# Kernel tuning notes

Measured on AMD Instinct MI355X. Metric: run time of the kernel, lower is better.

Reference implementation:

```python
import jax, jax.numpy as jnp
import numpy as np

D_MODEL = 768
D_STATE = 16
D_CONV = 4
EXPAND = 2
D_IN = D_MODEL // 2          # per-direction model dim = 384
D_INNER = EXPAND * D_IN      # ssm inner dim = 768
DT_RANK = (D_IN + 15) // 16  # 24 (mamba 'auto')
B, L = 2, 2048
EPS = 1e-5


def silu(x):
    return x * jax.nn.sigmoid(x)


def layernorm(x, w, b):
    m = jnp.mean(x, axis=-1, keepdims=True)
    v = jnp.var(x, axis=-1, keepdims=True)
    return (x - m) * jax.lax.rsqrt(v + EPS) * w + b


def causal_conv1d(u, w, b):
    # u: (B,L,di), w: (di,K) depthwise causal conv, b: (di,)
    K = w.shape[1]
    up = jnp.pad(u, ((0, 0), (K - 1, 0), (0, 0)))
    Lq = u.shape[1]
    y = sum(up[:, k:k + Lq, :] * w[:, k] for k in range(K))
    return y + b


def mamba_ssm(u, in_w, in_b, conv_w, conv_b, xp_w, dt_w, dt_b, A_log, Dp, out_w, out_b):
    # u: (B,L,D_IN)
    Bz = u.shape[0]
    xz = u @ in_w + in_b                         # (B,L,2*D_INNER)
    x, z = jnp.split(xz, 2, axis=-1)             # (B,L,D_INNER) each
    x = silu(causal_conv1d(x, conv_w, conv_b))
    xd = x @ xp_w                                # (B,L,DT_RANK+2N)
    dt = jax.nn.softplus(xd[..., :DT_RANK] @ dt_w + dt_b)   # (B,L,D_INNER)
    Bm = xd[..., DT_RANK:DT_RANK + D_STATE]      # (B,L,N)
    Cm = xd[..., DT_RANK + D_STATE:]             # (B,L,N)
    A = -jnp.exp(A_log)                          # (D_INNER,N)

    def step(h, xs):
        dt_t, x_t, B_t, C_t = xs                 # (B,di),(B,di),(B,N),(B,N)
        h = jnp.exp(dt_t[..., None] * A) * h + (dt_t * x_t)[..., None] * B_t[:, None, :]
        y = jnp.einsum('bdn,bn->bd', h, C_t)
        return h, y

    h0 = jnp.zeros((Bz, D_INNER, D_STATE), x.dtype)
    xs = (dt.transpose(1, 0, 2), x.transpose(1, 0, 2),
          Bm.transpose(1, 0, 2), Cm.transpose(1, 0, 2))
    _, ys = jax.lax.scan(step, h0, xs)           # ys: (L,B,D_INNER)
    y = ys.transpose(1, 0, 2) + x * Dp
    y = y * silu(z)
    return y @ out_w + out_b                     # (B,L,D_IN)


def setup_inputs() -> dict:
    key = jax.random.key(0)

    def nrm(i, shape, s=0.02):
        return jax.random.normal(jax.random.fold_in(key, i), shape, jnp.float32) * s

    d = {"x": jax.random.normal(jax.random.fold_in(key, 0), (B, L, D_MODEL), jnp.float32)}
    d["in_norm_w"] = jnp.ones(D_MODEL); d["in_norm_b"] = jnp.zeros(D_MODEL)
    d["ip_w"] = nrm(1, (D_MODEL, 2 * D_IN)); d["ip_b"] = jnp.zeros(2 * D_IN)
    i = 10
    for p in ("f", "b"):
        d[p + "_in_w"] = nrm(i, (D_IN, 2 * D_INNER)); d[p + "_in_b"] = jnp.zeros(2 * D_INNER)
        d[p + "_conv_w"] = nrm(i + 1, (D_INNER, D_CONV), 0.2); d[p + "_conv_b"] = jnp.zeros(D_INNER)
        d[p + "_xp_w"] = nrm(i + 2, (D_INNER, DT_RANK + 2 * D_STATE))
        d[p + "_dt_w"] = nrm(i + 3, (DT_RANK, D_INNER), 0.1)
        d[p + "_dt_b"] = nrm(i + 4, (D_INNER,), 0.5)
        d[p + "_A_log"] = jnp.log(jnp.tile(jnp.arange(1, D_STATE + 1, dtype=jnp.float32), (D_INNER, 1)))
        d[p + "_D"] = jnp.ones(D_INNER)
        d[p + "_out_w"] = nrm(i + 5, (D_INNER, D_IN)); d[p + "_out_b"] = jnp.zeros(D_IN)
        i += 10
    d["op_w"] = nrm(30, (2 * D_IN, D_MODEL)); d["op_b"] = jnp.zeros(D_MODEL)
    d["norm_w"] = jnp.ones(D_MODEL); d["norm_b"] = jnp.zeros(D_MODEL)
    return d


def reference(x, in_norm_w, in_norm_b, ip_w, ip_b,
              f_in_w, f_in_b, f_conv_w, f_conv_b, f_xp_w, f_dt_w, f_dt_b, f_A_log, f_D, f_out_w, f_out_b,
              b_in_w, b_in_b, b_conv_w, b_conv_b, b_xp_w, b_dt_w, b_dt_b, b_A_log, b_D, b_out_w, b_out_b,
              op_w, op_b, norm_w, norm_b):
    residual = x
    xn = layernorm(x, in_norm_w, in_norm_b)
    xp = xn @ ip_w + ip_b                        # (B,L,2*D_IN)
    x_fwd, x_bwd = jnp.split(xp, 2, axis=-1)
    out_fwd = mamba_ssm(x_fwd, f_in_w, f_in_b, f_conv_w, f_conv_b, f_xp_w,
                        f_dt_w, f_dt_b, f_A_log, f_D, f_out_w, f_out_b)
    out_bwd = mamba_ssm(jnp.flip(x_bwd, axis=1), b_in_w, b_in_b, b_conv_w, b_conv_b, b_xp_w,
                        b_dt_w, b_dt_b, b_A_log, b_D, b_out_w, b_out_b)
    out_bwd = jnp.flip(out_bwd, axis=1)
    out = jnp.concatenate([out_fwd, out_bwd], axis=-1) @ op_w + op_b
    # dropout is identity in eval mode
    return layernorm(residual + out, norm_w, norm_b)
```

## Files before the change

kernel.cpp:

```cpp
#include <hip/hip_runtime.h>
#include <hip/hip_bf16.h>
#include <math.h>
#include <type_traits>

#define BATCH 2
#define SEQ   2048
#define DMODEL 768
#define DIN   384
#define DINNER 768
#define DSTATE 16
#define DTRANK 24
#define ROWS  (BATCH*SEQ)
#define NCH   64
#define CLEN  (SEQ/NCH)

using short8  = __attribute__((ext_vector_type(8))) short;
using floatx4 = __attribute__((ext_vector_type(4))) float;

__device__ __forceinline__ ushort f2bf(float f) {
    union { float f; uint u; } v; v.f = f;
    uint r = (v.u + 0x7fffu + ((v.u >> 16) & 1u)) >> 16;
    return (ushort)r;
}
__device__ __forceinline__ float bf2f(ushort h) {
    union { uint u; float f; } v; v.u = ((uint)h) << 16;
    return v.f;
}
__device__ __forceinline__ void async16(const ushort* g, ushort* l) {
    __builtin_amdgcn_global_load_lds(
        (const __attribute__((address_space(1))) void*)g,
        (__attribute__((address_space(3))) void*)l,
        16, 0, 0);
}

template<int TM, int TN> struct GemmShT { ushort lA[TM * 64]; ushort lB[TN * 64]; };

template<int TM, int TN>
__device__ __forceinline__ void gemm_accum(
    const ushort* __restrict__ A, int lda,
    const ushort* __restrict__ Bt, int ldb,
    int K, int m0, int n0, GemmShT<TM, TN>& sh,
    floatx4 (&acc)[TM / 32][TN / 32])
{
    constexpr int WM = TM / 2, WN = TN / 2;
    constexpr int MT = WM / 16, NT = WN / 16;
    constexpr int AI = TM / 32, BI = TN / 32;
    const int tid = threadIdx.x;
    const int wave = tid >> 6, lane = tid & 63;
    const int wm = wave >> 1, wn = wave & 1;
    const int quad = lane >> 4, l16 = lane & 15;
    const int lrow = lane >> 3;
    const int lcol = ((lane & 7) ^ (lane >> 3)) * 8;

    for (int k0 = 0; k0 < K; k0 += 64) {
#pragma unroll
        for (int i = 0; i < AI; i++) {
            int rb = (wave * AI + i) * 8;
            async16(A + (size_t)(m0 + rb + lrow) * lda + k0 + lcol, &sh.lA[rb * 64]);
        }
#pragma unroll
        for (int i = 0; i < BI; i++) {
            int rb = (wave * BI + i) * 8;
            async16(Bt + (size_t)(n0 + rb + lrow) * ldb + k0 + lcol, &sh.lB[rb * 64]);
        }
        __syncthreads();
#pragma unroll
        for (int ks = 0; ks < 2; ks++) {
            short8 af[MT], bf[NT];
#pragma unroll
            for (int i = 0; i < MT; i++) {
                int row = wm * WM + i * 16 + l16;
                af[i] = *(const short8*)&sh.lA[row * 64 + ((ks * 4 + quad) ^ (row & 7)) * 8];
            }
#pragma unroll
            for (int j = 0; j < NT; j++) {
                int row = wn * WN + j * 16 + l16;
                bf[j] = *(const short8*)&sh.lB[row * 64 + ((ks * 4 + quad) ^ (row & 7)) * 8];
            }
#pragma unroll
            for (int i = 0; i < MT; i++)
#pragma unroll
                for (int j = 0; j < NT; j++)
                    acc[i][j] = __builtin_amdgcn_mfma_f32_16x16x32_bf16(af[i], bf[j], acc[i][j], 0, 0, 0);
        }
        __syncthreads();
    }
}

template<int TM, int TN, bool OUT_BF>
__device__ __forceinline__ void gemm_epilogue(
    const float* __restrict__ bias, void* __restrict__ C, int ldc, int N,
    int m0, int n0, floatx4 (&acc)[TM / 32][TN / 32])
{
    constexpr int WM = TM / 2, WN = TN / 2;
    constexpr int MT = WM / 16, NT = WN / 16;
    const int tid = threadIdx.x;
    const int wave = tid >> 6, lane = tid & 63;
    const int wm = wave >> 1, wn = wave & 1;
    const int quad = lane >> 4, l16 = lane & 15;
#pragma unroll
    for (int i = 0; i < MT; i++) {
#pragma unroll
        for (int j = 0; j < NT; j++) {
            int row = m0 + wm * WM + i * 16 + quad * 4;
            int col = n0 + wn * WN + j * 16 + l16;
            if (col < N) {
                float bv = bias ? bias[col] : 0.f;
#pragma unroll
                for (int r = 0; r < 4; r++) {
                    float v = acc[i][j][r] + bv;
                    if (OUT_BF) ((ushort*)C)[(size_t)(row + r) * ldc + col] = f2bf(v);
                    else        ((float*)C)[(size_t)(row + r) * ldc + col] = v;
                }
            }
        }
    }
}

template<int TM, int TN, bool OUT_BF>
__global__ __launch_bounds__(256) void mfma_gemm_k(
    const ushort* __restrict__ A0, const ushort* __restrict__ A1, int lda,
    const ushort* __restrict__ B0, const ushort* __restrict__ B1, int ldb,
    const float* __restrict__ bias0, const float* __restrict__ bias1,
    void* __restrict__ C0, void* __restrict__ C1, int ldc, int N, int K)
{
    __shared__ GemmShT<TM, TN> sh;
    const ushort* A  = blockIdx.z ? A1 : A0;
    const ushort* Bt = blockIdx.z ? B1 : B0;
    const float* bias = blockIdx.z ? bias1 : bias0;
    void* C = blockIdx.z ? C1 : C0;
    floatx4 acc[TM / 32][TN / 32];
#pragma unroll
    for (int i = 0; i < TM / 32; i++)
#pragma unroll
        for (int j = 0; j < TN / 32; j++)
            acc[i][j] = (floatx4){0.f, 0.f, 0.f, 0.f};
    int m0 = blockIdx.y * TM, n0 = blockIdx.x * TN;
    gemm_accum<TM, TN>(A, lda, Bt, ldb, K, m0, n0, sh, acc);
    gemm_epilogue<TM, TN, OUT_BF>(bias, C, ldc, N, m0, n0, acc);
}

__global__ __launch_bounds__(256) void xddt_kernel(
    const ushort* __restrict__ xcf, const ushort* __restrict__ xcb,
    const ushort* __restrict__ Wcf, const ushort* __restrict__ Wcb,
    const float* __restrict__ dtbf, const float* __restrict__ dtbb,
    float* __restrict__ xdf, float* __restrict__ xdb,
    float* __restrict__ dtf, float* __restrict__ dtb)
{
    constexpr int TM = 128, TN = 64;
    __shared__ GemmShT<TM, TN> sh;
    const ushort* A  = blockIdx.z ? xcb : xcf;
    const ushort* Bt = blockIdx.z ? Wcb : Wcf;
    const float* dbias = blockIdx.z ? dtbb : dtbf;
    float* xd = blockIdx.z ? xdb : xdf;
    float* dt = blockIdx.z ? dtb : dtf;
    floatx4 acc[4][2];
#pragma unroll
    for (int i = 0; i < 4; i++)
#pragma unroll
        for (int j = 0; j < 2; j++)
            acc[i][j] = (floatx4){0.f, 0.f, 0.f, 0.f};
    int m0 = blockIdx.y * TM, n0 = blockIdx.x * TN;
    gemm_accum<TM, TN>(A, 768, Bt, 768, 768, m0, n0, sh, acc);
    const int tid = threadIdx.x;
    const int wave = tid >> 6, lane = tid & 63;
    const int wm = wave >> 1, wn = wave & 1;
    const int quad = lane >> 4, l16 = lane & 15;
#pragma unroll
    for (int i = 0; i < 4; i++) {
#pragma unroll
        for (int j = 0; j < 2; j++) {
            int row = m0 + wm * 64 + i * 16 + quad * 4;
            int col = n0 + wn * 32 + j * 16 + l16;
            if (col < 56) {
#pragma unroll
                for (int r = 0; r < 4; r++)
                    xd[(size_t)(row + r) * 56 + col] = acc[i][j][r];
            } else if (col >= 64) {
                int jj = col - 64;
                float bv = dbias[jj];
#pragma unroll
                for (int r = 0; r < 4; r++) {
                    float v = acc[i][j][r] + bv;
                    v = (v > 20.f) ? v : log1pf(__expf(v));
                    dt[(size_t)(row + r) * 768 + jj] = v;
                }
            }
        }
    }
}

template<int TM, int TN>
__global__ __launch_bounds__(256) void outop_kernel(
    const ushort* __restrict__ A0, const ushort* __restrict__ B0,
    const ushort* __restrict__ A1, const ushort* __restrict__ B1,
    const float* __restrict__ bias, float* __restrict__ C,
    int lda, int ldb, int ldc, int N, int K)
{
    __shared__ GemmShT<TM, TN> sh;
    floatx4 acc[TM / 32][TN / 32];
#pragma unroll
    for (int i = 0; i < TM / 32; i++)
#pragma unroll
        for (int j = 0; j < TN / 32; j++)
            acc[i][j] = (floatx4){0.f, 0.f, 0.f, 0.f};
    int m0 = blockIdx.y * TM, n0 = blockIdx.x * TN;
    gemm_accum<TM, TN>(A0, lda, B0, ldb, K, m0, n0, sh, acc);
    gemm_accum<TM, TN>(A1, lda, B1, ldb, K, m0, n0, sh, acc);
    gemm_epilogue<TM, TN, false>(bias, (void*)C, ldc, N, m0, n0, acc);
}

struct LnSh { float ss[4]; float ssq[4]; float m; float rs; };

template<bool OUT_BF>
__device__ __forceinline__ void ln_row(
    int row, const float* __restrict__ x, const float* __restrict__ res,
    const float* __restrict__ w, const float* __restrict__ b,
    void* __restrict__ out, LnSh& sh)
{
    int tid = threadIdx.x;
    const float* xr = x + (size_t)row * DMODEL;
    const float* rr = res ? res + (size_t)row * DMODEL : nullptr;
    float v[3];
    float s = 0.f, sq = 0.f;
#pragma unroll
    for (int j = 0; j < 3; j++) {
        int i = tid + j * 256;
        float val = xr[i];
        if (rr) val += rr[i];
        v[j] = val; s += val; sq += val * val;
    }
#pragma unroll
    for (int off = 32; off; off >>= 1) {
        s  += __shfl_down(s,  off);
        sq += __shfl_down(sq, off);
    }
    int wid = tid >> 6;
    if ((tid & 63) == 0) { sh.ss[wid] = s; sh.ssq[wid] = sq; }
    __syncthreads();
    if (tid == 0) {
        float S  = sh.ss[0] + sh.ss[1] + sh.ss[2] + sh.ss[3];
        float SQ = sh.ssq[0] + sh.ssq[1] + sh.ssq[2] + sh.ssq[3];
        float m  = S * (1.0f / DMODEL);
        float var = SQ * (1.0f / DMODEL) - m * m;
        sh.m = m;
        sh.rs = rsqrtf(var + 1e-5f);
    }
    __syncthreads();
    float m = sh.m, rs = sh.rs;
#pragma unroll
    for (int j = 0; j < 3; j++) {
        int i = tid + j * 256;
        float r = (v[j] - m) * rs * w[i] + b[i];
        if (OUT_BF) ((ushort*)out)[(size_t)row * DMODEL + i] = f2bf(r);
        else        ((float*)out)[(size_t)row * DMODEL + i] = r;
    }
}

__global__ __launch_bounds__(256) void ln2_kernel(
    const float* __restrict__ x, const float* __restrict__ res,
    const float* __restrict__ w, const float* __restrict__ b,
    float* __restrict__ out)
{
    __shared__ LnSh sh;
    ln_row<false>(blockIdx.x, x, res, w, b, (void*)out, sh);
}

struct TD { const float* src; ushort* dst; int K, N, Kp, Np, ldd, tile0, tkp, mode; };
struct PrepArgs {
    TD d[12];
    int ntc;
    const float *x, *in_nw, *in_nb;
    ushort* xn;
};

__global__ __launch_bounds__(256) void prep_kernel(PrepArgs p)
{
    __shared__ union { float tile[32][33]; LnSh l; } sh;
    int bi = blockIdx.x;
    if (bi < p.ntc) {
        int i = 0;
        while (i < 11 && bi >= p.d[i + 1].tile0) i++;
        TD t = p.d[i];
        int local = bi - t.tile0;
        int tki = local % t.tkp, tn = local / t.tkp;
        int k0 = tki * 32, n0 = tn * 32;
        if (t.mode == 0) {
            int tx = threadIdx.x & 31, ty = threadIdx.x >> 5;
#pragma unroll
            for (int r = ty; r < 32; r += 8) {
                int k = k0 + r, n = n0 + tx;
                sh.tile[r][tx] = (k < t.K && n < t.N) ? t.src[(size_t)k * t.N + n] : 0.f;
            }
            __syncthreads();
#pragma unroll
            for (int r = ty; r < 32; r += 8) {
                int n = n0 + r, k = k0 + tx;
                t.dst[(size_t)n * t.ldd + k] = f2bf(sh.tile[tx][r]);
            }
        } else {
#pragma unroll
            for (int e = threadIdx.x; e < 1024; e += 256) {
                int r = e >> 5, c = e & 31;
                int k = k0 + r, n = n0 + c;
                float v = (k < t.K && n < t.N) ? t.src[(size_t)k * t.N + n] : 0.f;
                t.dst[(size_t)k * t.ldd + n] = f2bf(v);
            }
        }
    } else {
        ln_row<true>(bi - p.ntc, p.x, (const float*)nullptr, p.in_nw, p.in_nb,
                     (void*)p.xn, sh.l);
    }
}

struct WfArgs {
    const ushort *fin, *bin, *opT, *ipc, *fow, *bow;
    const ushort *dtwTf, *dtwTb, *xpcf, *xpcb;
    ushort *WzF, *WzB, *WoF, *WoB, *WcF, *WcB;
    const float *ip_b, *f_in_b, *b_in_b, *f_out_b, *b_out_b, *op_b;
    const float *f_in_w32, *b_in_w32, *op_w32;
    float *bzf, *bzb, *bo;
};

__global__ __launch_bounds__(256) void wfuse_kernel(WfArgs p)
{
    __shared__ GemmShT<128, 64> sh;
    int t = blockIdx.x;
    if (t < 576) {
        const ushort *A, *Bt; ushort* C; int lda, ldb, K, m0, n0;
        if (t < 144)      { A = p.fin;   lda = 384; Bt = p.ipc;       ldb = 768; K = 384; C = p.WzF;           int u = t;       m0 = (u / 12) * 128; n0 = (u % 12) * 64; }
        else if (t < 288) { A = p.bin;   lda = 384; Bt = p.ipc + 384; ldb = 768; K = 384; C = p.WzB;           int u = t - 144; m0 = (u / 12) * 128; n0 = (u % 12) * 64; }
        else if (t < 360) { A = p.opT;   lda = 768; Bt = p.fow;       ldb = 384; K = 384; C = p.WoF;           int u = t - 288; m0 = (u / 12) * 128; n0 = (u % 12) * 64; }
        else if (t < 432) { A = p.opT + 384; lda = 768; Bt = p.bow;   ldb = 384; K = 384; C = p.WoB;           int u = t - 360; m0 = (u / 12) * 128; n0 = (u % 12) * 64; }
        else if (t < 504) { A = p.dtwTf; lda = 64;  Bt = p.xpcf;      ldb = 64;  K = 64;  C = p.WcF + 64*768;  int u = t - 432; m0 = (u / 12) * 128; n0 = (u % 12) * 64; }
        else              { A = p.dtwTb; lda = 64;  Bt = p.xpcb;      ldb = 64;  K = 64;  C = p.WcB + 64*768;  int u = t - 504; m0 = (u / 12) * 128; n0 = (u % 12) * 64; }
        floatx4 acc[4][2];
#pragma unroll
        for (int i = 0; i < 4; i++)
#pragma unroll
            for (int j = 0; j < 2; j++)
                acc[i][j] = (floatx4){0.f, 0.f, 0.f, 0.f};
        gemm_accum<128, 64>(A, lda, Bt, ldb, K, m0, n0, sh, acc);
        gemm_epilogue<128, 64, true>((const float*)nullptr, (void*)C, 768, 768, m0, n0, acc);
    } else if (t < 582) {
        int n = (t - 576) * 256 + threadIdx.x;
        float acc = p.f_in_b[n];
        for (int j = 0; j < 384; j++)
            acc = fmaf(p.ip_b[j], p.f_in_w32[(size_t)j * 1536 + n], acc);
        p.bzf[n] = acc;
    } else if (t < 588) {
        int n = (t - 582) * 256 + threadIdx.x;
        float acc = p.b_in_b[n];
        for (int j = 0; j < 384; j++)
            acc = fmaf(p.ip_b[384 + j], p.b_in_w32[(size_t)j * 1536 + n], acc);
        p.bzb[n] = acc;
    } else {
        int n = (t - 588) * 256 + threadIdx.x;
        float acc = p.op_b[n];
        for (int j = 0; j < 384; j++)
            acc = fmaf(p.f_out_b[j], p.op_w32[(size_t)j * 768 + n], acc);
        for (int j = 0; j < 384; j++)
            acc = fmaf(p.b_out_b[j], p.op_w32[(size_t)(384 + j) * 768 + n], acc);
        p.bo[n] = acc;
    }
}

__global__ __launch_bounds__(256) void conv_silu_kernel(
    const ushort* __restrict__ xzf, const ushort* __restrict__ xzb,
    const float* __restrict__ cwf, const float* __restrict__ cbf,
    const float* __restrict__ cwb, const float* __restrict__ cbb,
    ushort* __restrict__ outf, ushort* __restrict__ outb)
{
    int rev = blockIdx.y;
    const ushort* xz = rev ? xzb : xzf;
    const float* cw = rev ? cwb : cwf;
    const float* cb = rev ? cbb : cbf;
    ushort* out = rev ? outb : outf;

    int idx = blockIdx.x * 256 + threadIdx.x;
    int d = idx % DINNER;
    int row = idx / DINNER;
    int t = row & (SEQ - 1), b = row >> 11;
    float4 w4 = *(const float4*)&cw[d * 4];
    float wk[4] = {w4.x, w4.y, w4.z, w4.w};
    float acc = cb[d];
#pragma unroll
    for (int k = 0; k < 4; k++) {
        int ts = rev ? (t + 3 - k) : (t - 3 + k);
        if (ts >= 0 && ts < SEQ)
            acc = fmaf(wk[k], bf2f(xz[((size_t)(b * SEQ + ts)) * 1536 + d]), acc);
    }
    float sig = 1.f / (1.f + __expf(-acc));
    out[idx] = f2bf(acc * sig);
}

template<bool FULL>
__global__ __launch_bounds__(256) void scan_chunk_kernel(
    const float* __restrict__ dtf, const ushort* __restrict__ xcf,
    const float* __restrict__ xdf, const ushort* __restrict__ xzf,
    const float* __restrict__ Alf, const float* __restrict__ Dff,
    const float* __restrict__ dtb, const ushort* __restrict__ xcb,
    const float* __restrict__ xdb, const ushort* __restrict__ xzb,
    const float* __restrict__ Alb, const float* __restrict__ Dbb,
    float* __restrict__ Hloc, float* __restrict__ Wp,
    const float* __restrict__ Hin,
    ushort* __restrict__ yf, ushort* __restrict__ yb)
{
    const int d     = blockIdx.x * 256 + threadIdx.x;
    const int chunk = blockIdx.y;
    const int bz    = blockIdx.z;
    const int dir   = bz >> 1;
    const int bat   = bz & 1;

    const float*  dt = dir ? dtb : dtf;
    const ushort* xc = dir ? xcb : xcf;
    const float*  xd = dir ? xdb : xdf;
    const ushort* xz = dir ? xzb : xzf;
    const float*  Al = dir ? Alb : Alf;
    const float*  Dp = dir ? Dbb : Dff;
    ushort* yo = dir ? yb : yf;

    float a[16];
    {
        const float4* Ap = (const float4*)(Al + (size_t)d * 16);
#pragma unroll
        for (int q = 0; q < 4; q++) {
            float4 v = Ap[q];
            a[q*4+0] = -__expf(v.x); a[q*4+1] = -__expf(v.y);
            a[q*4+2] = -__expf(v.z); a[q*4+3] = -__expf(v.w);
        }
    }
    const float a0 = a[0];
    bool fast = true;
#pragma unroll
    for (int n = 0; n < 16; n++) {
        float ideal = a0 * (float)(n + 1);
        fast = fast && (fabsf(a[n] - ideal) <= 1e-4f * fabsf(ideal) + 1e-7f);
    }

    float h[16];
    if (FULL) {
        size_t base = ((size_t)(bz * NCH + chunk) * DINNER + d) * 16;
#pragma unroll
        for (int q = 0; q < 4; q++) {
            float4 v = *(const float4*)(Hin + base + q * 4);
            h[q*4+0] = v.x; h[q*4+1] = v.y; h[q*4+2] = v.z; h[q*4+3] = v.w;
        }
    } else {
#pragma unroll
        for (int n = 0; n < 16; n++) h[n] = 0.f;
    }

    const float Dd = FULL ? Dp[d] : 0.f;
    float S = 0.f;

    auto run = [&](auto FASTC) {
        constexpr bool FAST = decltype(FASTC)::value;
#pragma unroll 2
        for (int i = 0; i < CLEN; i++) {
            int tl = chunk * CLEN + i;
            int t  = dir ? (SEQ - 1 - tl) : tl;
            size_t r = (size_t)(bat * SEQ + t);
            float dtv = dt[r * DINNER + d];
            float xv  = bf2f(xc[r * DINNER + d]);
            const float* bp = xd + r * 56 + DTRANK;
            float4 B0 = *(const float4*)(bp + 0);
            float4 B1 = *(const float4*)(bp + 4);
            float4 B2 = *(const float4*)(bp + 8);
            float4 B3 = *(const float4*)(bp + 12);
            float Bv[16] = {B0.x,B0.y,B0.z,B0.w, B1.x,B1.y,B1.z,B1.w,
                            B2.x,B2.y,B2.z,B2.w, B3.x,B3.y,B3.z,B3.w};
            float w[16];
            if (FAST) {
                float e1 = __expf(dtv * a0);
                float e2 = e1*e1, e4 = e2*e2, e8 = e4*e4;
                w[0]=e1;      w[1]=e2;      w[2]=e2*e1;   w[3]=e4;
                w[4]=e4*e1;   w[5]=e4*e2;   w[6]=e4*w[2]; w[7]=e8;
                w[8]=e8*e1;   w[9]=e8*e2;   w[10]=e8*w[2];w[11]=e8*e4;
                w[12]=e8*w[4];w[13]=e8*w[5];w[14]=e8*w[6];w[15]=e8*e8;
            } else {
#pragma unroll
                for (int n = 0; n < 16; n++) w[n] = __expf(dtv * a[n]);
            }
            float bx = dtv * xv;
#pragma unroll
            for (int n = 0; n < 16; n++)
                h[n] = fmaf(w[n], h[n], bx * Bv[n]);
            S += dtv;
            if (FULL) {
                const float* cp = bp + DSTATE;
                float4 C0 = *(const float4*)(cp + 0);
                float4 C1 = *(const float4*)(cp + 4);
                float4 C2 = *(const float4*)(cp + 8);
                float4 C3 = *(const float4*)(cp + 12);
                float Cv[16] = {C0.x,C0.y,C0.z,C0.w, C1.x,C1.y,C1.z,C1.w,
                                C2.x,C2.y,C2.z,C2.w, C3.x,C3.y,C3.z,C3.w};
                float y = 0.f;
#pragma unroll
                for (int n = 0; n < 16; n++) y = fmaf(h[n], Cv[n], y);
                float zv = bf2f(xz[r * 1536 + DINNER + d]);
                float sig = 1.f / (1.f + __expf(-zv));
                yo[r * DINNER + d] = f2bf((y + xv * Dd) * (zv * sig));
            }
        }
    };
    if (fast) run(std::true_type{}); else run(std::false_type{});

    if (!FULL) {
        float W[16];
        if (fast) {
            float E1 = __expf(S * a0);
            float E2 = E1*E1, E4 = E2*E2, E8 = E4*E4;
            W[0]=E1;      W[1]=E2;      W[2]=E2*E1;   W[3]=E4;
            W[4]=E4*E1;   W[5]=E4*E2;   W[6]=E4*W[2]; W[7]=E8;
            W[8]=E8*E1;   W[9]=E8*E2;   W[10]=E8*W[2];W[11]=E8*E4;
            W[12]=E8*W[4];W[13]=E8*W[5];W[14]=E8*W[6];W[15]=E8*E8;
        } else {
#pragma unroll
            for (int n = 0; n < 16; n++) W[n] = __expf(S * a[n]);
        }
        size_t base = ((size_t)(bz * NCH + chunk) * DINNER + d) * 16;
#pragma unroll
        for (int q = 0; q < 4; q++) {
            *(float4*)(Hloc + base + q*4) = make_float4(h[q*4+0], h[q*4+1], h[q*4+2], h[q*4+3]);
            *(float4*)(Wp   + base + q*4) = make_float4(W[q*4+0], W[q*4+1], W[q*4+2], W[q*4+3]);
        }
    }
}

__global__ __launch_bounds__(256) void scan_combine(
    const float* __restrict__ Hloc, const float* __restrict__ Wp,
    float* __restrict__ Hin)
{
    int idx = blockIdx.x * 256 + threadIdx.x;
    int bz = idx / (DINNER * 16);
    int rest = idx % (DINNER * 16);
    float hin = 0.f;
#pragma unroll 4
    for (int k = 0; k < NCH; k++) {
        size_t o = (size_t)(bz * NCH + k) * (DINNER * 16) + rest;
        Hin[o] = hin;
        hin = fmaf(Wp[o], hin, Hloc[o]);
    }
}

extern "C" void kernel_launch(void* const* d_in, const int* in_sizes, int n_in,
                              void* d_out, int out_size, void* d_ws, size_t ws_size,
                              hipStream_t stream)
{
    const float* x        = (const float*)d_in[0];
    const float* in_nw    = (const float*)d_in[1];
    const float* in_nb    = (const float*)d_in[2];
    const float* ip_w     = (const float*)d_in[3];
    const float* ip_b     = (const float*)d_in[4];
    const float* f_in_w   = (const float*)d_in[5];
    const float* f_in_b   = (const float*)d_in[6];
    const float* f_conv_w = (const float*)d_in[7];
    const float* f_conv_b = (const float*)d_in[8];
    const float* f_xp_w   = (const float*)d_in[9];
    const float* f_dt_w   = (const float*)d_in[10];
    const float* f_dt_b   = (const float*)d_in[11];
    const float* f_A_log  = (const float*)d_in[12];
    const float* f_D      = (const float*)d_in[13];
    const float* f_out_w  = (const float*)d_in[14];
    const float* f_out_b  = (const float*)d_in[15];
    const float* b_in_w   = (const float*)d_in[16];
    const float* b_in_b   = (const float*)d_in[17];
    const float* b_conv_w = (const float*)d_in[18];
    const float* b_conv_b = (const float*)d_in[19];
    const float* b_xp_w   = (const float*)d_in[20];
    const float* b_dt_w   = (const float*)d_in[21];
    const float* b_dt_b   = (const float*)d_in[22];
    const float* b_A_log  = (const float*)d_in[23];
    const float* b_D      = (const float*)d_in[24];
    const float* b_out_w  = (const float*)d_in[25];
    const float* b_out_b  = (const float*)d_in[26];
    const float* op_w     = (const float*)d_in[27];
    const float* op_b     = (const float*)d_in[28];
    const float* norm_w   = (const float*)d_in[29];
    const float* norm_b   = (const float*)d_in[30];

    size_t off = 0;
    auto alloc = [&](size_t bytes) {
        void* p = (char*)d_ws + off;
        off += (bytes + 255) & ~(size_t)255;
        return p;
    };
    const size_t R = ROWS;
    ushort* xn_bf   = (ushort*)alloc(R * 768 * 2);
    ushort* xz_f_bf = (ushort*)alloc(R * 1536 * 2);
    ushort* xz_b_bf = (ushort*)alloc(R * 1536 * 2);
    ushort* xc_f_bf = (ushort*)alloc(R * 768 * 2);
    ushort* xc_b_bf = (ushort*)alloc(R * 768 * 2);
    float*  xd_f    = (float*)alloc(R * 56 * 4);
    float*  xd_b    = (float*)alloc(R * 56 * 4);
    float*  dt_f    = (float*)alloc(R * 768 * 4);
    float*  dt_b    = (float*)alloc(R * 768 * 4);
    ushort* y_f_bf  = (ushort*)alloc(R * 768 * 2);
    ushort* y_b_bf  = (ushort*)alloc(R * 768 * 2);
    float*  outraw  = (float*)alloc(R * 768 * 4);
    const size_t SCN = (size_t)4 * NCH * DINNER * 16;
    float* Hloc = (float*)alloc(SCN * 4);
    float* Wpb  = (float*)alloc(SCN * 4);
    float* Hin  = (float*)alloc(SCN * 4);
    ushort* Wt_fin = (ushort*)alloc((size_t)1536 * 384 * 2);
    ushort* Wt_bin = (ushort*)alloc((size_t)1536 * 384 * 2);
    ushort* Wt_op  = (ushort*)alloc((size_t)768 * 768 * 2);
    ushort* ipc    = (ushort*)alloc((size_t)768 * 768 * 2);
    ushort* fow    = (ushort*)alloc((size_t)768 * 384 * 2);
    ushort* bow    = (ushort*)alloc((size_t)768 * 384 * 2);
    ushort* dtwT_f = (ushort*)alloc((size_t)768 * 64 * 2);
    ushort* dtwT_b = (ushort*)alloc((size_t)768 * 64 * 2);
    ushort* xpc_f  = (ushort*)alloc((size_t)768 * 64 * 2);
    ushort* xpc_b  = (ushort*)alloc((size_t)768 * 64 * 2);
    ushort* WzF    = (ushort*)alloc((size_t)1536 * 768 * 2);
    ushort* WzB    = (ushort*)alloc((size_t)1536 * 768 * 2);
    ushort* WoF    = (ushort*)alloc((size_t)768 * 768 * 2);
    ushort* WoB    = (ushort*)alloc((size_t)768 * 768 * 2);
    ushort* WcF    = (ushort*)alloc((size_t)832 * 768 * 2);
    ushort* WcB    = (ushort*)alloc((size_t)832 * 768 * 2);
    float*  bzf    = (float*)alloc(1536 * 4);
    float*  bzb    = (float*)alloc(1536 * 4);
    float*  bo     = (float*)alloc(768 * 4);

    PrepArgs pa;
    int tile0 = 0, nd = 0;
    auto add = [&](const float* s, ushort* dst, int K, int N, int Kp, int Np,
                   int ldd, int mode) {
        pa.d[nd] = TD{s, dst, K, N, Kp, Np, ldd, tile0, Kp / 32, mode};
        tile0 += (Kp / 32) * (Np / 32);
        nd++;
    };
    add(f_in_w,  Wt_fin,      384, 1536, 384, 1536, 384, 0);
    add(b_in_w,  Wt_bin,      384, 1536, 384, 1536, 384, 0);
    add(op_w,    Wt_op,       768, 768,  768, 768,  768, 0);
    add(f_xp_w,  WcF,         768, 56,   768, 64,   768, 0);
    add(b_xp_w,  WcB,         768, 56,   768, 64,   768, 0);
    add(f_dt_w,  dtwT_f,      24,  768,  64,  768,  64,  0);
    add(b_dt_w,  dtwT_b,      24,  768,  64,  768,  64,  0);
    add(ip_w,    ipc,         768, 768,  768, 768,  768, 1);
    add(f_out_w, fow,         768, 384,  768, 384,  384, 1);
    add(b_out_w, bow,         768, 384,  768, 384,  384, 1);
    add(f_xp_w,  xpc_f,       768, 56,   768, 64,   64,  1);
    add(b_xp_w,  xpc_b,       768, 56,   768, 64,   64,  1);
    pa.ntc = tile0;
    pa.x = x; pa.in_nw = in_nw; pa.in_nb = in_nb; pa.xn = xn_bf;
    hipLaunchKernelGGL(prep_kernel, dim3(tile0 + ROWS), dim3(256), 0, stream, pa);

    WfArgs wa;
    wa.fin = Wt_fin; wa.bin = Wt_bin; wa.opT = Wt_op;
    wa.ipc = ipc; wa.fow = fow; wa.bow = bow;
    wa.dtwTf = dtwT_f; wa.dtwTb = dtwT_b; wa.xpcf = xpc_f; wa.xpcb = xpc_b;
    wa.WzF = WzF; wa.WzB = WzB; wa.WoF = WoF; wa.WoB = WoB; wa.WcF = WcF; wa.WcB = WcB;
    wa.ip_b = ip_b; wa.f_in_b = f_in_b; wa.b_in_b = b_in_b;
    wa.f_out_b = f_out_b; wa.b_out_b = b_out_b; wa.op_b = op_b;
    wa.f_in_w32 = f_in_w; wa.b_in_w32 = b_in_w; wa.op_w32 = op_w;
    wa.bzf = bzf; wa.bzb = bzb; wa.bo = bo;
    hipLaunchKernelGGL(wfuse_kernel, dim3(591), dim3(256), 0, stream, wa);

    hipLaunchKernelGGL((mfma_gemm_k<128, 128, true>), dim3(12, 32, 2), dim3(256), 0, stream,
                       xn_bf, xn_bf, 768, WzF, WzB, 768, bzf, bzb,
                       (void*)xz_f_bf, (void*)xz_b_bf, 1536, 1536, 768);

    hipLaunchKernelGGL(conv_silu_kernel, dim3(ROWS * DINNER / 256, 2), dim3(256), 0, stream,
                       xz_f_bf, xz_b_bf, f_conv_w, f_conv_b, b_conv_w, b_conv_b,
                       xc_f_bf, xc_b_bf);

    hipLaunchKernelGGL(xddt_kernel, dim3(13, 32, 2), dim3(256), 0, stream,
                       xc_f_bf, xc_b_bf, WcF, WcB, f_dt_b, b_dt_b,
                       xd_f, xd_b, dt_f, dt_b);

    hipLaunchKernelGGL((scan_chunk_kernel<false>), dim3(DINNER / 256, NCH, 4), dim3(256), 0, stream,
                       dt_f, xc_f_bf, xd_f, xz_f_bf, f_A_log, f_D,
                       dt_b, xc_b_bf, xd_b, xz_b_bf, b_A_log, b_D,
                       Hloc, Wpb, (const float*)nullptr, (ushort*)nullptr, (ushort*)nullptr);
    hipLaunchKernelGGL(scan_combine, dim3(4 * DINNER * 16 / 256), dim3(256), 0, stream,
                       Hloc, Wpb, Hin);
    hipLaunchKernelGGL((scan_chunk_kernel<true>), dim3(DINNER / 256, NCH, 4), dim3(256), 0, stream,
                       dt_f, xc_f_bf, xd_f, xz_f_bf, f_A_log, f_D,
                       dt_b, xc_b_bf, xd_b, xz_b_bf, b_A_log, b_D,
                       (float*)nullptr, (float*)nullptr, Hin, y_f_bf, y_b_bf);

    hipLaunchKernelGGL((outop_kernel<128, 64>), dim3(12, 32), dim3(256), 0, stream,
                       y_f_bf, WoF, y_b_bf, WoB, bo, outraw, 768, 768, 768, 768, 768);

    hipLaunchKernelGGL(ln2_kernel, dim3(ROWS), dim3(256), 0, stream,
                       x, outraw, norm_w, norm_b, (float*)d_out);
}
```

Before: 364.9 us.

## Unfuse x_proj and dt_proj into two GEMMs with bf16 intermediate

The earlier code pre-multiplied dt_w into x_proj weights (a 768x768 folded matrix per direction) so one K=768 GEMM produced both xd and dt. Now x_proj runs as its own small GEMM (N=64) writing bf16 xd, and a separate K=64 GEMM computes dt from it with a numerically stable softplus. This removes the large folded-weight precompute and cuts the main GEMM's work from about 832x768 to 64x768 plus 768x64 per row. In exchange it adds a kernel launch, routes dt through a bf16-rounded intermediate, and has the scan read B and C as bf16, which lowers precision.

```diff
diff --git a/kernel.cpp b/kernel.cpp
--- a/kernel.cpp
+++ b/kernel.cpp
@@ -32,6 +32,11 @@
         (__attribute__((address_space(3))) void*)l,
         16, 0, 0);
 }
+__device__ __forceinline__ float softplus_fast(float v) {
+    if (v > 20.f) return v;
+    float e = __expf(-fabsf(v));
+    return fmaxf(v, 0.f) + __logf(1.f + e);
+}
 
 template<int TM, int TN> struct GemmShT { ushort lA[TM * 64]; ushort lB[TN * 64]; };
 
@@ -140,20 +145,18 @@
     gemm_epilogue<TM, TN, OUT_BF>(bias, C, ldc, N, m0, n0, acc);
 }
 
-__global__ __launch_bounds__(256) void xddt_kernel(
-    const ushort* __restrict__ xcf, const ushort* __restrict__ xcb,
-    const ushort* __restrict__ Wcf, const ushort* __restrict__ Wcb,
+__global__ __launch_bounds__(256) void dt_kernel(
+    const ushort* __restrict__ xdf, const ushort* __restrict__ xdb,
+    const ushort* __restrict__ dtwTf, const ushort* __restrict__ dtwTb,
     const float* __restrict__ dtbf, const float* __restrict__ dtbb,
-    float* __restrict__ xdf, float* __restrict__ xdb,
     float* __restrict__ dtf, float* __restrict__ dtb)
 {
     constexpr int TM = 128, TN = 64;
     __shared__ GemmShT<TM, TN> sh;
-    const ushort* A  = blockIdx.z ? xcb : xcf;
-    const ushort* Bt = blockIdx.z ? Wcb : Wcf;
-    const float* dbias = blockIdx.z ? dtbb : dtbf;
-    float* xd = blockIdx.z ? xdb : xdf;
-    float* dt = blockIdx.z ? dtb : dtf;
+    const ushort* A  = blockIdx.z ? xdb : xdf;
+    const ushort* Bt = blockIdx.z ? dtwTb : dtwTf;
+    const float* bias = blockIdx.z ? dtbb : dtbf;
+    float* C = blockIdx.z ? dtb : dtf;
     floatx4 acc[4][2];
 #pragma unroll
     for (int i = 0; i < 4; i++)
@@ -161,7 +164,7 @@
         for (int j = 0; j < 2; j++)
             acc[i][j] = (floatx4){0.f, 0.f, 0.f, 0.f};
     int m0 = blockIdx.y * TM, n0 = blockIdx.x * TN;
-    gemm_accum<TM, TN>(A, 768, Bt, 768, 768, m0, n0, sh, acc);
+    gemm_accum<TM, TN>(A, 64, Bt, 64, 64, m0, n0, sh, acc);
     const int tid = threadIdx.x;
     const int wave = tid >> 6, lane = tid & 63;
     const int wm = wave >> 1, wn = wave & 1;
@@ -172,20 +175,10 @@
         for (int j = 0; j < 2; j++) {
             int row = m0 + wm * 64 + i * 16 + quad * 4;
             int col = n0 + wn * 32 + j * 16 + l16;
-            if (col < 56) {
-#pragma unroll
-                for (int r = 0; r < 4; r++)
-                    xd[(size_t)(row + r) * 56 + col] = acc[i][j][r];
-            } else if (col >= 64) {
-                int jj = col - 64;
-                float bv = dbias[jj];
-#pragma unroll
-                for (int r = 0; r < 4; r++) {
-                    float v = acc[i][j][r] + bv;
-                    v = (v > 20.f) ? v : log1pf(__expf(v));
-                    dt[(size_t)(row + r) * 768 + jj] = v;
-                }
-            }
+            float bv = bias[col];
+#pragma unroll
+            for (int r = 0; r < 4; r++)
+                C[(size_t)(row + r) * 768 + col] = softplus_fast(acc[i][j][r] + bv);
         }
     }
 }
@@ -315,8 +308,7 @@
 
 struct WfArgs {
     const ushort *fin, *bin, *opT, *ipc, *fow, *bow;
-    const ushort *dtwTf, *dtwTb, *xpcf, *xpcb;
-    ushort *WzF, *WzB, *WoF, *WoB, *WcF, *WcB;
+    ushort *WzF, *WzB, *WoF, *WoB;
     const float *ip_b, *f_in_b, *b_in_b, *f_out_b, *b_out_b, *op_b;
     const float *f_in_w32, *b_in_w32, *op_w32;
     float *bzf, *bzb, *bo;
@@ -326,36 +318,34 @@
 {
     __shared__ GemmShT<128, 64> sh;
     int t = blockIdx.x;
-    if (t < 576) {
-        const ushort *A, *Bt; ushort* C; int lda, ldb, K, m0, n0;
-        if (t < 144)      { A = p.fin;   lda = 384; Bt = p.ipc;       ldb = 768; K = 384; C = p.WzF;           int u = t;       m0 = (u / 12) * 128; n0 = (u % 12) * 64; }
-        else if (t < 288) { A = p.bin;   lda = 384; Bt = p.ipc + 384; ldb = 768; K = 384; C = p.WzB;           int u = t - 144; m0 = (u / 12) * 128; n0 = (u % 12) * 64; }
-        else if (t < 360) { A = p.opT;   lda = 768; Bt = p.fow;       ldb = 384; K = 384; C = p.WoF;           int u = t - 288; m0 = (u / 12) * 128; n0 = (u % 12) * 64; }
-        else if (t < 432) { A = p.opT + 384; lda = 768; Bt = p.bow;   ldb = 384; K = 384; C = p.WoB;           int u = t - 360; m0 = (u / 12) * 128; n0 = (u % 12) * 64; }
-        else if (t < 504) { A = p.dtwTf; lda = 64;  Bt = p.xpcf;      ldb = 64;  K = 64;  C = p.WcF + 64*768;  int u = t - 432; m0 = (u / 12) * 128; n0 = (u % 12) * 64; }
-        else              { A = p.dtwTb; lda = 64;  Bt = p.xpcb;      ldb = 64;  K = 64;  C = p.WcB + 64*768;  int u = t - 504; m0 = (u / 12) * 128; n0 = (u % 12) * 64; }
+    if (t < 432) {
+        const ushort *A, *Bt; ushort* C; int lda, ldb, m0, n0;
+        if (t < 144)      { A = p.fin;       lda = 384; Bt = p.ipc;       ldb = 768; C = p.WzF; int u = t;       m0 = (u / 12) * 128; n0 = (u % 12) * 64; }
+        else if (t < 288) { A = p.bin;       lda = 384; Bt = p.ipc + 384; ldb = 768; C = p.WzB; int u = t - 144; m0 = (u / 12) * 128; n0 = (u % 12) * 64; }
+        else if (t < 360) { A = p.opT;       lda = 768; Bt = p.fow;       ldb = 384; C = p.WoF; int u = t - 288; m0 = (u / 12) * 128; n0 = (u % 12) * 64; }
+        else              { A = p.opT + 384; lda = 768; Bt = p.bow;       ldb = 384; C = p.WoB; int u = t - 360; m0 = (u / 12) * 128; n0 = (u % 12) * 64; }
         floatx4 acc[4][2];
 #pragma unroll
         for (int i = 0; i < 4; i++)
 #pragma unroll
             for (int j = 0; j < 2; j++)
                 acc[i][j] = (floatx4){0.f, 0.f, 0.f, 0.f};
-        gemm_accum<128, 64>(A, lda, Bt, ldb, K, m0, n0, sh, acc);
+        gemm_accum<128, 64>(A, lda, Bt, ldb, 384, m0, n0, sh, acc);
         gemm_epilogue<128, 64, true>((const float*)nullptr, (void*)C, 768, 768, m0, n0, acc);
-    } else if (t < 582) {
-        int n = (t - 576) * 256 + threadIdx.x;
+    } else if (t < 438) {
+        int n = (t - 432) * 256 + threadIdx.x;
         float acc = p.f_in_b[n];
         for (int j = 0; j < 384; j++)
             acc = fmaf(p.ip_b[j], p.f_in_w32[(size_t)j * 1536 + n], acc);
         p.bzf[n] = acc;
-    } else if (t < 588) {
-        int n = (t - 582) * 256 + threadIdx.x;
+    } else if (t < 444) {
+        int n = (t - 438) * 256 + threadIdx.x;
         float acc = p.b_in_b[n];
         for (int j = 0; j < 384; j++)
             acc = fmaf(p.ip_b[384 + j], p.b_in_w32[(size_t)j * 1536 + n], acc);
         p.bzb[n] = acc;
     } else {
-        int n = (t - 588) * 256 + threadIdx.x;
+        int n = (t - 444) * 256 + threadIdx.x;
         float acc = p.op_b[n];
         for (int j = 0; j < 384; j++)
             acc = fmaf(p.f_out_b[j], p.op_w32[(size_t)j * 768 + n], acc);
@@ -397,10 +387,10 @@
 template<bool FULL>
 __global__ __launch_bounds__(256) void scan_chunk_kernel(
     const float* __restrict__ dtf, const ushort* __restrict__ xcf,
-    const float* __restrict__ xdf, const ushort* __restrict__ xzf,
+    const ushort* __restrict__ xdf, const ushort* __restrict__ xzf,
     const float* __restrict__ Alf, const float* __restrict__ Dff,
     const float* __restrict__ dtb, const ushort* __restrict__ xcb,
-    const float* __restrict__ xdb, const ushort* __restrict__ xzb,
+    const ushort* __restrict__ xdb, const ushort* __restrict__ xzb,
     const float* __restrict__ Alb, const float* __restrict__ Dbb,
     float* __restrict__ Hloc, float* __restrict__ Wp,
     const float* __restrict__ Hin,
@@ -414,7 +404,7 @@
 
     const float*  dt = dir ? dtb : dtf;
     const ushort* xc = dir ? xcb : xcf;
-    const float*  xd = dir ? xdb : xdf;
+    const ushort* xd = dir ? xdb : xdf;
     const ushort* xz = dir ? xzb : xzf;
     const float*  Al = dir ? Alb : Alf;
     const float*  Dp = dir ? Dbb : Dff;
@@ -463,13 +453,15 @@
             size_t r = (size_t)(bat * SEQ + t);
             float dtv = dt[r * DINNER + d];
             float xv  = bf2f(xc[r * DINNER + d]);
-            const float* bp = xd + r * 56 + DTRANK;
-            float4 B0 = *(const float4*)(bp + 0);
-            float4 B1 = *(const float4*)(bp + 4);
-            float4 B2 = *(const float4*)(bp + 8);
-            float4 B3 = *(const float4*)(bp + 12);
-            float Bv[16] = {B0.x,B0.y,B0.z,B0.w, B1.x,B1.y,B1.z,B1.w,
-                            B2.x,B2.y,B2.z,B2.w, B3.x,B3.y,B3.z,B3.w};
+            const ushort* bp = xd + r * 64 + DTRANK;
+            short8 b0 = *(const short8*)(bp);
+            short8 b1 = *(const short8*)(bp + 8);
+            float Bv[16];
+#pragma unroll
+            for (int n = 0; n < 8; n++) {
+                Bv[n]     = bf2f((ushort)b0[n]);
+                Bv[8 + n] = bf2f((ushort)b1[n]);
+            }
             float w[16];
             if (FAST) {
                 float e1 = __expf(dtv * a0);
@@ -488,13 +480,14 @@
                 h[n] = fmaf(w[n], h[n], bx * Bv[n]);
             S += dtv;
             if (FULL) {
-                const float* cp = bp + DSTATE;
-                float4 C0 = *(const float4*)(cp + 0);
-                float4 C1 = *(const float4*)(cp + 4);
-                float4 C2 = *(const float4*)(cp + 8);
-                float4 C3 = *(const float4*)(cp + 12);
-                float Cv[16] = {C0.x,C0.y,C0.z,C0.w, C1.x,C1.y,C1.z,C1.w,
-                                C2.x,C2.y,C2.z,C2.w, C3.x,C3.y,C3.z,C3.w};
+                short8 c0 = *(const short8*)(bp + 16);
+                short8 c1 = *(const short8*)(bp + 24);
+                float Cv[16];
+#pragma unroll
+                for (int n = 0; n < 8; n++) {
+                    Cv[n]     = bf2f((ushort)c0[n]);
+                    Cv[8 + n] = bf2f((ushort)c1[n]);
+                }
                 float y = 0.f;
 #pragma unroll
                 for (int n = 0; n < 16; n++) y = fmaf(h[n], Cv[n], y);
@@ -592,8 +585,8 @@
     ushort* xz_b_bf = (ushort*)alloc(R * 1536 * 2);
     ushort* xc_f_bf = (ushort*)alloc(R * 768 * 2);
     ushort* xc_b_bf = (ushort*)alloc(R * 768 * 2);
-    float*  xd_f    = (float*)alloc(R * 56 * 4);
-    float*  xd_b    = (float*)alloc(R * 56 * 4);
+    ushort* xd64_f  = (ushort*)alloc(R * 64 * 2);
+    ushort* xd64_b  = (ushort*)alloc(R * 64 * 2);
     float*  dt_f    = (float*)alloc(R * 768 * 4);
     float*  dt_b    = (float*)alloc(R * 768 * 4);
     ushort* y_f_bf  = (ushort*)alloc(R * 768 * 2);
@@ -606,19 +599,17 @@
     ushort* Wt_fin = (ushort*)alloc((size_t)1536 * 384 * 2);
     ushort* Wt_bin = (ushort*)alloc((size_t)1536 * 384 * 2);
     ushort* Wt_op  = (ushort*)alloc((size_t)768 * 768 * 2);
+    ushort* Wt_fxp = (ushort*)alloc((size_t)64 * 768 * 2);
+    ushort* Wt_bxp = (ushort*)alloc((size_t)64 * 768 * 2);
+    ushort* dtwT_f = (ushort*)alloc((size_t)768 * 64 * 2);
+    ushort* dtwT_b = (ushort*)alloc((size_t)768 * 64 * 2);
     ushort* ipc    = (ushort*)alloc((size_t)768 * 768 * 2);
     ushort* fow    = (ushort*)alloc((size_t)768 * 384 * 2);
     ushort* bow    = (ushort*)alloc((size_t)768 * 384 * 2);
-    ushort* dtwT_f = (ushort*)alloc((size_t)768 * 64 * 2);
-    ushort* dtwT_b = (ushort*)alloc((size_t)768 * 64 * 2);
-    ushort* xpc_f  = (ushort*)alloc((size_t)768 * 64 * 2);
-    ushort* xpc_b  = (ushort*)alloc((size_t)768 * 64 * 2);
     ushort* WzF    = (ushort*)alloc((size_t)1536 * 768 * 2);
     ushort* WzB    = (ushort*)alloc((size_t)1536 * 768 * 2);
     ushort* WoF    = (ushort*)alloc((size_t)768 * 768 * 2);
     ushort* WoB    = (ushort*)alloc((size_t)768 * 768 * 2);
-    ushort* WcF    = (ushort*)alloc((size_t)832 * 768 * 2);
-    ushort* WcB    = (ushort*)alloc((size_t)832 * 768 * 2);
     float*  bzf    = (float*)alloc(1536 * 4);
     float*  bzb    = (float*)alloc(1536 * 4);
     float*  bo     = (float*)alloc(768 * 4);
@@ -631,32 +622,30 @@
         tile0 += (Kp / 32) * (Np / 32);
         nd++;
     };
-    add(f_in_w,  Wt_fin,      384, 1536, 384, 1536, 384, 0);
-    add(b_in_w,  Wt_bin,      384, 1536, 384, 1536, 384, 0);
-    add(op_w,    Wt_op,       768, 768,  768, 768,  768, 0);
-    add(f_xp_w,  WcF,         768, 56,   768, 64,   768, 0);
-    add(b_xp_w,  WcB,         768, 56,   768, 64,   768, 0);
-    add(f_dt_w,  dtwT_f,      24,  768,  64,  768,  64,  0);
-    add(b_dt_w,  dtwT_b,      24,  768,  64,  768,  64,  0);
-    add(ip_w,    ipc,         768, 768,  768, 768,  768, 1);
-    add(f_out_w, fow,         768, 384,  768, 384,  384, 1);
-    add(b_out_w, bow,         768, 384,  768, 384,  384, 1);
-    add(f_xp_w,  xpc_f,       768, 56,   768, 64,   64,  1);
-    add(b_xp_w,  xpc_b,       768, 56,   768, 64,   64,  1);
+    add(f_in_w,  Wt_fin, 384, 1536, 384, 1536, 384, 0);
+    add(b_in_w,  Wt_bin, 384, 1536, 384, 1536, 384, 0);
+    add(op_w,    Wt_op,  768, 768,  768, 768,  768, 0);
+    add(f_xp_w,  Wt_fxp, 768, 56,   768, 64,   768, 0);
+    add(b_xp_w,  Wt_bxp, 768, 56,   768, 64,   768, 0);
+    add(f_dt_w,  dtwT_f, 24,  768,  64,  768,  64,  0);
+    add(b_dt_w,  dtwT_b, 24,  768,  64,  768,  64,  0);
+    add(ip_w,    ipc,    768, 768,  768, 768,  768, 1);
+    add(f_out_w, fow,    768, 384,  768, 384,  384, 1);
+    add(b_out_w, bow,    768, 384,  768, 384,  384, 1);
     pa.ntc = tile0;
+    for (int i = nd; i < 12; i++) pa.d[i].tile0 = 0x7fffffff;
     pa.x = x; pa.in_nw = in_nw; pa.in_nb = in_nb; pa.xn = xn_bf;
     hipLaunchKernelGGL(prep_kernel, dim3(tile0 + ROWS), dim3(256), 0, stream, pa);
 
     WfArgs wa;
     wa.fin = Wt_fin; wa.bin = Wt_bin; wa.opT = Wt_op;
     wa.ipc = ipc; wa.fow = fow; wa.bow = bow;
-    wa.dtwTf = dtwT_f; wa.dtwTb = dtwT_b; wa.xpcf = xpc_f; wa.xpcb = xpc_b;
-    wa.WzF = WzF; wa.WzB = WzB; wa.WoF = WoF; wa.WoB = WoB; wa.WcF = WcF; wa.WcB = WcB;
+    wa.WzF = WzF; wa.WzB = WzB; wa.WoF = WoF; wa.WoB = WoB;
     wa.ip_b = ip_b; wa.f_in_b = f_in_b; wa.b_in_b = b_in_b;
     wa.f_out_b = f_out_b; wa.b_out_b = b_out_b; wa.op_b = op_b;
     wa.f_in_w32 = f_in_w; wa.b_in_w32 = b_in_w; wa.op_w32 = op_w;
     wa.bzf = bzf; wa.bzb = bzb; wa.bo = bo;
-    hipLaunchKernelGGL(wfuse_kernel, dim3(591), dim3(256), 0, stream, wa);
+    hipLaunchKernelGGL(wfuse_kernel, dim3(447), dim3(256), 0, stream, wa);
 
     hipLaunchKernelGGL((mfma_gemm_k<128, 128, true>), dim3(12, 32, 2), dim3(256), 0, stream,
                        xn_bf, xn_bf, 768, WzF, WzB, 768, bzf, bzb,
@@ -666,19 +655,23 @@
                        xz_f_bf, xz_b_bf, f_conv_w, f_conv_b, b_conv_w, b_conv_b,
                        xc_f_bf, xc_b_bf);
 
-    hipLaunchKernelGGL(xddt_kernel, dim3(13, 32, 2), dim3(256), 0, stream,
-                       xc_f_bf, xc_b_bf, WcF, WcB, f_dt_b, b_dt_b,
-                       xd_f, xd_b, dt_f, dt_b);
+    hipLaunchKernelGGL((mfma_gemm_k<64, 64, true>), dim3(1, 64, 2), dim3(256), 0, stream,
+                       xc_f_bf, xc_b_bf, 768, Wt_fxp, Wt_bxp, 768,
+                       (const float*)nullptr, (const float*)nullptr,
+                       (void*)xd64_f, (void*)xd64_b, 64, 64, 768);
+
+    hipLaunchKernelGGL(dt_kernel, dim3(12, 32, 2), dim3(256), 0, stream,
+                       xd64_f, xd64_b, dtwT_f, dtwT_b, f_dt_b, b_dt_b, dt_f, dt_b);
 
     hipLaunchKernelGGL((scan_chunk_kernel<false>), dim3(DINNER / 256, NCH, 4), dim3(256), 0, stream,
-                       dt_f, xc_f_bf, xd_f, xz_f_bf, f_A_log, f_D,
-                       dt_b, xc_b_bf, xd_b, xz_b_bf, b_A_log, b_D,
+                       dt_f, xc_f_bf, xd64_f, xz_f_bf, f_A_log, f_D,
+                       dt_b, xc_b_bf, xd64_b, xz_b_bf, b_A_log, b_D,
                        Hloc, Wpb, (const float*)nullptr, (ushort*)nullptr, (ushort*)nullptr);
     hipLaunchKernelGGL(scan_combine, dim3(4 * DINNER * 16 / 256), dim3(256), 0, stream,
                        Hloc, Wpb, Hin);
     hipLaunchKernelGGL((scan_chunk_kernel<true>), dim3(DINNER / 256, NCH, 4), dim3(256), 0, stream,
-                       dt_f, xc_f_bf, xd_f, xz_f_bf, f_A_log, f_D,
-                       dt_b, xc_b_bf, xd_b, xz_b_bf, b_A_log, b_D,
+                       dt_f, xc_f_bf, xd64_f, xz_f_bf, f_A_log, f_D,
+                       dt_b, xc_b_bf, xd64_b, xz_b_bf, b_A_log, b_D,
                        (float*)nullptr, (float*)nullptr, Hin, y_f_bf, y_b_bf);
 
     hipLaunchKernelGGL((outop_kernel<128, 64>), dim3(12, 32), dim3(256), 0, stream,
```

Result: faster. 331.5 us (-9.1%).
